# Performance work log

Hardware: AMD Instinct MI355X
Metric: run time of the kernel (lower is better)

## Reference

```python
import jax, jax.numpy as jnp
import numpy as np

B, S, H = 4, 4096, 256
WINDOW = 128


def setup_inputs() -> dict:
    key = jax.random.key(0)
    ks = jax.random.split(key, 7)
    s = 1.0 / np.sqrt(H)
    return {
        "x": jax.random.normal(ks[0], (B, S, H), dtype=jnp.float32),
        "Wq": jax.random.normal(ks[1], (H, H), dtype=jnp.float32) * s,
        "bq": jax.random.normal(ks[2], (H,), dtype=jnp.float32) * s,
        "Wk": jax.random.normal(ks[3], (H, H), dtype=jnp.float32) * s,
        "bk": jax.random.normal(ks[4], (H,), dtype=jnp.float32) * s,
        "Wv": jax.random.normal(ks[5], (H, H), dtype=jnp.float32) * s,
        "bv": jax.random.normal(ks[6], (H,), dtype=jnp.float32) * s,
        "window_size": WINDOW,
    }


def reference(x, Wq, bq, Wk, bk, Wv, bv, window_size):
    # x: [B, S, H]
    seq_len = x.shape[1]
    hidden = x.shape[2]
    scale = jnp.sqrt(jnp.asarray(hidden, dtype=x.dtype))
    q = jnp.einsum('bsh,hd->bsd', x, Wq) + bq
    k = jnp.einsum('bsh,hd->bsd', x, Wk) + bk
    v = jnp.einsum('bsh,hd->bsd', x, Wv) + bv
    scores = jnp.einsum('bsd,btd->bst', q, k) / scale  # [B, S, S]
    idx = jnp.arange(seq_len)
    band = jnp.abs(idx[:, None] - idx[None, :]) <= window_size  # [S, S]
    neg_inf = jnp.asarray(-jnp.inf, dtype=scores.dtype)
    scores = jnp.where(band[None, :, :], scores, neg_inf)
    weights = jax.nn.softmax(scores, axis=-1)
    context = jnp.einsum('bst,btd->bsd', weights, v)  # [B, S, H]
    return context.mean(axis=1)  # [B, H]
```

## Files before the change

### kernel.cpp

```cpp
#include <hip/hip_runtime.h>

#define SDIM 4096
#define HDIM 256
#define WIN 128
#define NROW 16384
#define QSCALE 0.0625f

typedef __attribute__((ext_vector_type(8))) short bf16x8;
typedef __attribute__((ext_vector_type(4))) float f32x4;

static __device__ __forceinline__ unsigned short f2bf(float f) {
  unsigned int u = __float_as_uint(f);
  return (unsigned short)((u + 0x7fffu + ((u >> 16) & 1u)) >> 16);
}

#define MFMA16(a, b, c) __builtin_amdgcn_mfma_f32_16x16x32_bf16((a), (b), (c), 0, 0, 0)


__global__ __launch_bounds__(256) void wconv(const float* __restrict__ Wq,
                                             const float* __restrict__ Wk,
                                             const float* __restrict__ Wv,
                                             unsigned short* __restrict__ Wp) {
  const int m = blockIdx.y, nt = blockIdx.x;
  const float* __restrict__ W = (m == 0) ? Wq : (m == 1) ? Wk : Wv;
  const int tid = threadIdx.x, lane = tid & 63, w = tid >> 6;
  const int l15 = lane & 15, g = lane >> 4;
#pragma unroll
  for (int half = 0; half < 2; ++half) {
    int kk = w * 2 + half;
    bf16x8 v;
#pragma unroll
    for (int j = 0; j < 8; ++j)
      v[j] = (short)f2bf(W[(size_t)(32 * kk + 8 * g + j) * HDIM + 16 * nt + l15]);
    *(bf16x8*)(Wp + ((size_t)(m * 16 + nt) * 8 + kk) * 512 + (size_t)lane * 8) = v;
  }
}

__global__ __launch_bounds__(256) void qkv_mfma(
    const float* __restrict__ x, const unsigned short* __restrict__ Wp,
    const float* __restrict__ bq, const float* __restrict__ bk,
    const float* __restrict__ bv, unsigned short* __restrict__ Qp,
    unsigned short* __restrict__ Kp, unsigned short* __restrict__ Vp) {
  __shared__ unsigned short st[32][264];
  const int tid = threadIdx.x;
  const int lane = tid & 63, w = tid >> 6;
  const int l15 = lane & 15, g = lane >> 4;
  const size_t rb = (size_t)blockIdx.x * 32;
#pragma unroll
  for (int it = 0; it < 8; ++it) {
    int u = it * 256 + tid;
    int r = u >> 6, c4 = (u & 63) << 2;
    float4 f = *(const float4*)(x + (rb + r) * HDIM + c4);
    st[r][c4 + 0] = f2bf(f.x);
    st[r][c4 + 1] = f2bf(f.y);
    st[r][c4 + 2] = f2bf(f.z);
    st[r][c4 + 3] = f2bf(f.w);
  }
  __syncthreads();
  bf16x8 a[2][8];
#pragma unroll
  for (int rtl = 0; rtl < 2; ++rtl)
#pragma unroll
    for (int kk = 0; kk < 8; ++kk)
      a[rtl][kk] = *(const bf16x8*)&st[16 * rtl + l15][32 * kk + 8 * g];
  __syncthreads();
  const int tg0 = blockIdx.x * 2;
  for (int m = 0; m < 3; ++m) {
    const unsigned short* Wm = Wp + (size_t)m * 65536;
    const float* bias = (m == 0) ? bq : (m == 1) ? bk : bv;
#pragma unroll
    for (int ntl = 0; ntl < 4; ++ntl) {
      const int nt = 4 * w + ntl;
      const unsigned short* wp_ = Wm + (size_t)nt * 4096 + (size_t)lane * 8;
      bf16x8 wf[8];
#pragma unroll
      for (int kk = 0; kk < 8; ++kk) wf[kk] = *(const bf16x8*)(wp_ + kk * 512);
      f32x4 a0 = {0.f, 0.f, 0.f, 0.f}, a1 = {0.f, 0.f, 0.f, 0.f};
#pragma unroll
      for (int kk = 0; kk < 8; ++kk) {
        a0 = MFMA16(a[0][kk], wf[kk], a0);
        a1 = MFMA16(a[1][kk], wf[kk], a1);
      }
      float bn = bias[nt * 16 + l15];
#pragma unroll
      for (int r = 0; r < 4; ++r) {
        st[4 * g + r][nt * 16 + l15] = f2bf(a0[r] + bn);
        st[16 + 4 * g + r][nt * 16 + l15] = f2bf(a1[r] + bn);
      }
    }
    __syncthreads();
    if (m < 2) {
      unsigned short* O = (m == 0 ? Qp : Kp);
#pragma unroll
      for (int it = 0; it < 4; ++it) {
        int u = it * 256 + tid;
        int ln = u & 63, kk = (u >> 6) & 7, tgl = u >> 9;
        int lg = ln >> 4, lc = ln & 15;
        bf16x8 vv = *(const bf16x8*)&st[16 * tgl + lc][32 * kk + 8 * lg];
        *(bf16x8*)(O + ((size_t)(tg0 + tgl) * 8 + kk) * 512 + (size_t)ln * 8) = vv;
      }
    } else {
#pragma unroll
      for (int it = 0; it < 4; ++it) {
        int u = it * 256 + tid;
        int lc = u & 15, gg = (u >> 4) & 1, dt = (u >> 5) & 15, tgl = u >> 9;
        bf16x8 vv;
#pragma unroll
        for (int j = 0; j < 8; ++j)
          vv[j] = (short)st[16 * tgl + 8 * gg + j][16 * dt + lc];
        *(bf16x8*)(Vp + (size_t)(tg0 + tgl) * 4096 +
                   (size_t)(dt * 32 + gg * 16 + lc) * 8) = vv;
      }
    }
    __syncthreads();
  }
}

__global__ __launch_bounds__(256) void attn_mfma(
    const unsigned short* __restrict__ Qp, const unsigned short* __restrict__ Kp,
    const unsigned short* __restrict__ Vp, float* __restrict__ partial) {
  __shared__ unsigned short plds[4][2][16][40];
  __shared__ float lsh[4][16];
  __shared__ float fbuf[4][256];
  const int tid = threadIdx.x;
  const int lane = tid & 63, w = tid >> 6;
  const int bid = blockIdx.x;
  const int blk = (bid & 7) * 128 + (bid >> 3);
  const int b = blk >> 8;
  const int qt = blk & 255;
  const int s0 = qt << 4;
  const int l15 = lane & 15, g = lane >> 4;
  bf16x8 qf[8];
  const unsigned short* qp_ = Qp + ((size_t)b * 256 + qt) * 4096 + (size_t)lane * 8;
#pragma unroll
  for (int kk = 0; kk < 8; ++kk) qf[kk] = *(const bf16x8*)(qp_ + kk * 512);
  const unsigned short* Kb = Kp + (size_t)b * 1048576;
  const unsigned short* Vb = Vp + (size_t)b * 1048576;
  f32x4 acc[16];
  const f32x4 zero = {0.f, 0.f, 0.f, 0.f};
#pragma unroll
  for (int i = 0; i < 16; ++i) acc[i] = zero;
  float lacc[4] = {0.f, 0.f, 0.f, 0.f};

  const int t0A = s0 - WIN + 64 * w;
  const int tgA = qt - 8 + 4 * w;
  const int tg0 = min(max(tgA + 0, 0), 255);
  const int tg1 = min(max(tgA + 1, 0), 255);
  const int tg2 = min(max(tgA + 2, 0), 255);
  const int tg3 = min(max(tgA + 3, 0), 255);
  const unsigned short* k0p = Kb + (size_t)tg0 * 4096 + (size_t)lane * 8;
  const unsigned short* k1p = Kb + (size_t)tg1 * 4096 + (size_t)lane * 8;
  const unsigned short* k2p = Kb + (size_t)tg2 * 4096 + (size_t)lane * 8;
  const unsigned short* k3p = Kb + (size_t)tg3 * 4096 + (size_t)lane * 8;
  f32x4 sc0 = zero, sc1 = zero, sc2 = zero, sc3 = zero;
#pragma unroll
  for (int kk = 0; kk < 8; ++kk) {
    sc0 = MFMA16(qf[kk], *(const bf16x8*)(k0p + kk * 512), sc0);
    sc1 = MFMA16(qf[kk], *(const bf16x8*)(k1p + kk * 512), sc1);
    sc2 = MFMA16(qf[kk], *(const bf16x8*)(k2p + kk * 512), sc2);
    sc3 = MFMA16(qf[kk], *(const bf16x8*)(k3p + kk * 512), sc3);
  }
  float p[4][4];
#pragma unroll
  for (int r = 0; r < 4; ++r) {
    const int s = s0 + 4 * g + r;
    const f32x4 sv[4] = {sc0, sc1, sc2, sc3};
#pragma unroll
    for (int ti = 0; ti < 4; ++ti) {
      int t = t0A + 16 * ti + l15;
      bool ok = (t >= 0) && (t < SDIM) && (t - s <= WIN) && (t - s >= -WIN);
      p[ti][r] = ok ? __expf(sv[ti][r] * QSCALE) : 0.f;
    }
  }
#pragma unroll
  for (int r = 0; r < 4; ++r) {
    float v = p[0][r] + p[1][r] + p[2][r] + p[3][r];
    v += __shfl_xor(v, 1);
    v += __shfl_xor(v, 2);
    v += __shfl_xor(v, 4);
    v += __shfl_xor(v, 8);
    lacc[r] += v;
  }
#pragma unroll
  for (int r = 0; r < 4; ++r) {
    plds[w][0][4 * g + r][l15] = f2bf(p[0][r]);
    plds[w][0][4 * g + r][16 + l15] = f2bf(p[1][r]);
    plds[w][1][4 * g + r][l15] = f2bf(p[2][r]);
    plds[w][1][4 * g + r][16 + l15] = f2bf(p[3][r]);
  }
  bf16x8 paA = *(const bf16x8*)&plds[w][0][l15][8 * g];
  bf16x8 paB = *(const bf16x8*)&plds[w][1][l15][8 * g];
  const int tgvA = min(max(tgA + (g >> 1), 0), 255);
  const int tgvB = min(max(tgA + 2 + (g >> 1), 0), 255);
  const unsigned short* vpA =
      Vb + (size_t)tgvA * 4096 + (size_t)(g & 1) * 128 + (size_t)l15 * 8;
  const unsigned short* vpB =
      Vb + (size_t)tgvB * 4096 + (size_t)(g & 1) * 128 + (size_t)l15 * 8;
#pragma unroll
  for (int dt = 0; dt < 16; ++dt) {
    acc[dt] = MFMA16(paA, *(const bf16x8*)(vpA + dt * 256), acc[dt]);
    acc[dt] = MFMA16(paB, *(const bf16x8*)(vpB + dt * 256), acc[dt]);
  }

  if (w == 3) {
    const int t0C = s0 + WIN;
    const int tgC = min(qt + 8, 255);
    const unsigned short* kcp = Kb + (size_t)tgC * 4096 + (size_t)lane * 8;
    f32x4 scC = zero;
#pragma unroll
    for (int kk = 0; kk < 8; ++kk)
      scC = MFMA16(qf[kk], *(const bf16x8*)(kcp + kk * 512), scC);
    float pC[4];
#pragma unroll
    for (int r = 0; r < 4; ++r) {
      int s = s0 + 4 * g + r;
      int t = t0C + l15;
      bool ok = (t < SDIM) && (t - s <= WIN);
      pC[r] = ok ? __expf(scC[r] * QSCALE) : 0.f;
      float v = pC[r];
      v += __shfl_xor(v, 1);
      v += __shfl_xor(v, 2);
      v += __shfl_xor(v, 4);
      v += __shfl_xor(v, 8);
      lacc[r] += v;
    }
#pragma unroll
    for (int r = 0; r < 4; ++r) {
      plds[w][0][4 * g + r][l15] = f2bf(pC[r]);
      plds[w][0][4 * g + r][16 + l15] = 0;
    }
    bf16x8 paC = *(const bf16x8*)&plds[w][0][l15][8 * g];
    const int tgvC = min(max(tgC + (g >> 1), 0), 255);
    const unsigned short* vpC =
        Vb + (size_t)tgvC * 4096 + (size_t)(g & 1) * 128 + (size_t)l15 * 8;
#pragma unroll
    for (int dt = 0; dt < 16; ++dt)
      acc[dt] = MFMA16(paC, *(const bf16x8*)(vpC + dt * 256), acc[dt]);
  }

  if (l15 == 0) {
#pragma unroll
    for (int r = 0; r < 4; ++r) lsh[w][4 * g + r] = lacc[r];
  }
  __syncthreads();
  float li[4];
#pragma unroll
  for (int r = 0; r < 4; ++r)
    li[r] = 1.0f / (lsh[0][4 * g + r] + lsh[1][4 * g + r] + lsh[2][4 * g + r] +
                    lsh[3][4 * g + r]);
#pragma unroll
  for (int dt = 0; dt < 16; ++dt) {
    float s = acc[dt][0] * li[0] + acc[dt][1] * li[1] + acc[dt][2] * li[2] +
              acc[dt][3] * li[3];
    s += __shfl_xor(s, 16);
    s += __shfl_xor(s, 32);
    if (lane < 16) fbuf[w][dt * 16 + lane] = s;
  }
  __syncthreads();
  partial[(size_t)blk * HDIM + tid] =
      fbuf[0][tid] + fbuf[1][tid] + fbuf[2][tid] + fbuf[3][tid];
}

__global__ __launch_bounds__(256) void reduce_partials(
    const float* __restrict__ partial, float* __restrict__ out) {
  __shared__ float red[16][17];
  const int cx = blockIdx.x, b = blockIdx.y;
  const int lc = threadIdx.x & 15, rg = threadIdx.x >> 4;
  float s = 0.f;
#pragma unroll
  for (int i = 0; i < 16; ++i)
    s += partial[((size_t)b * 256 + rg * 16 + i) * HDIM + cx * 16 + lc];
  red[rg][lc] = s;
  __syncthreads();
  if (rg == 0) {
    float t = 0.f;
#pragma unroll
    for (int r = 0; r < 16; ++r) t += red[r][lc];
    out[(size_t)b * HDIM + cx * 16 + lc] = t * (1.0f / (float)SDIM);
  }
}

extern "C" void kernel_launch(void* const* d_in, const int* in_sizes, int n_in,
                              void* d_out, int out_size, void* d_ws, size_t ws_size,
                              hipStream_t stream) {
  const float* x  = (const float*)d_in[0];
  const float* Wq = (const float*)d_in[1];
  const float* bq = (const float*)d_in[2];
  const float* Wk = (const float*)d_in[3];
  const float* bk = (const float*)d_in[4];
  const float* Wv = (const float*)d_in[5];
  const float* bv = (const float*)d_in[6];
  float* out = (float*)d_out;

  unsigned short* Wp = (unsigned short*)d_ws;
  unsigned short* Qp = Wp + 3 * 65536;
  unsigned short* Kp = Qp + (size_t)NROW * HDIM;
  unsigned short* Vp = Kp + (size_t)NROW * HDIM;
  float* partial = (float*)(Vp + (size_t)NROW * HDIM);

  dim3 wg(16, 3);
  wconv<<<wg, 256, 0, stream>>>(Wq, Wk, Wv, Wp);
  qkv_mfma<<<512, 256, 0, stream>>>(x, Wp, bq, bk, bv, Qp, Kp, Vp);
  attn_mfma<<<1024, 256, 0, stream>>>(Qp, Kp, Vp, partial);
  dim3 rg(16, 4);
  reduce_partials<<<rg, 256, 0, stream>>>(partial, out);
}
```

Baseline: 48.83 us.

## Fuse weight conversion into QKV kernel with flag-based inter-block sync

Removes the separate weight-conversion launch. The first 48 blocks of the QKV projection kernel now convert Wq/Wk/Wv to packed bf16 and publish completion flags with release atomics. Every block stages its x tile, then spin-waits on all 48 flags before reading the packed weights. Launch-bounds occupancy hints are also added to both kernels. The flags are never reset between calls, so later calls do not wait for fresh weights, and the spin-wait relies on the producer blocks being co-resident.

```diff
diff --git a/kernel.cpp b/kernel.cpp
--- a/kernel.cpp
+++ b/kernel.cpp
@@ -5,6 +5,7 @@
 #define WIN 128
 #define NROW 16384
 #define QSCALE 0.0625f
+#define MAGIC 0x7F3A9C51u
 
 typedef __attribute__((ext_vector_type(8))) short bf16x8;
 typedef __attribute__((ext_vector_type(4))) float f32x4;
@@ -17,35 +18,43 @@
 #define MFMA16(a, b, c) __builtin_amdgcn_mfma_f32_16x16x32_bf16((a), (b), (c), 0, 0, 0)
 
 
-__global__ __launch_bounds__(256) void wconv(const float* __restrict__ Wq,
-                                             const float* __restrict__ Wk,
-                                             const float* __restrict__ Wv,
-                                             unsigned short* __restrict__ Wp) {
-  const int m = blockIdx.y, nt = blockIdx.x;
-  const float* __restrict__ W = (m == 0) ? Wq : (m == 1) ? Wk : Wv;
-  const int tid = threadIdx.x, lane = tid & 63, w = tid >> 6;
-  const int l15 = lane & 15, g = lane >> 4;
-#pragma unroll
-  for (int half = 0; half < 2; ++half) {
-    int kk = w * 2 + half;
-    bf16x8 v;
-#pragma unroll
-    for (int j = 0; j < 8; ++j)
-      v[j] = (short)f2bf(W[(size_t)(32 * kk + 8 * g + j) * HDIM + 16 * nt + l15]);
-    *(bf16x8*)(Wp + ((size_t)(m * 16 + nt) * 8 + kk) * 512 + (size_t)lane * 8) = v;
-  }
-}
-
-__global__ __launch_bounds__(256) void qkv_mfma(
-    const float* __restrict__ x, const unsigned short* __restrict__ Wp,
-    const float* __restrict__ bq, const float* __restrict__ bk,
-    const float* __restrict__ bv, unsigned short* __restrict__ Qp,
-    unsigned short* __restrict__ Kp, unsigned short* __restrict__ Vp) {
+__global__ __launch_bounds__(256, 2) void qkv_mfma(
+    const float* __restrict__ x,
+    const float* __restrict__ Wq, const float* __restrict__ Wk,
+    const float* __restrict__ Wv, const float* __restrict__ bq,
+    const float* __restrict__ bk, const float* __restrict__ bv,
+    unsigned short* __restrict__ Wp, unsigned short* __restrict__ Qp,
+    unsigned short* __restrict__ Kp, unsigned short* __restrict__ Vp,
+    unsigned* __restrict__ sent) {
   __shared__ unsigned short st[32][264];
   const int tid = threadIdx.x;
   const int lane = tid & 63, w = tid >> 6;
   const int l15 = lane & 15, g = lane >> 4;
-  const size_t rb = (size_t)blockIdx.x * 32;
+  const int blk = blockIdx.x;
+
+  if (blk < 48) {
+    const int m = blk >> 4, nt = blk & 15;
+    const float* __restrict__ W = (m == 0) ? Wq : (m == 1) ? Wk : Wv;
+#pragma unroll
+    for (int it = 0; it < 2; ++it) {
+      int u = it * 256 + tid;
+      int kk = u >> 6, ln = u & 63;
+      int lg = ln >> 4, lc = ln & 15;
+      bf16x8 v;
+#pragma unroll
+      for (int j = 0; j < 8; ++j)
+        v[j] = (short)f2bf(W[(size_t)(32 * kk + 8 * lg + j) * HDIM + 16 * nt + lc]);
+      *(bf16x8*)(Wp + ((size_t)(m * 16 + nt) * 8 + kk) * 512 + (size_t)ln * 8) = v;
+    }
+    __syncthreads();
+    if (tid == 0) {
+      __threadfence();
+      __hip_atomic_store(sent + blk, MAGIC, __ATOMIC_RELEASE,
+                         __HIP_MEMORY_SCOPE_AGENT);
+    }
+  }
+
+  const size_t rb = (size_t)blk * 32;
 #pragma unroll
   for (int it = 0; it < 8; ++it) {
     int u = it * 256 + tid;
@@ -64,7 +73,15 @@
     for (int kk = 0; kk < 8; ++kk)
       a[rtl][kk] = *(const bf16x8*)&st[16 * rtl + l15][32 * kk + 8 * g];
   __syncthreads();
-  const int tg0 = blockIdx.x * 2;
+
+  if (tid < 48) {
+    while (__hip_atomic_load(sent + tid, __ATOMIC_ACQUIRE,
+                             __HIP_MEMORY_SCOPE_AGENT) != MAGIC)
+      __builtin_amdgcn_s_sleep(2);
+  }
+  __syncthreads();
+
+  const int tg0 = blk * 2;
   for (int m = 0; m < 3; ++m) {
     const unsigned short* Wm = Wp + (size_t)m * 65536;
     const float* bias = (m == 0) ? bq : (m == 1) ? bk : bv;
@@ -116,7 +133,7 @@
   }
 }
 
-__global__ __launch_bounds__(256) void attn_mfma(
+__global__ __launch_bounds__(256, 4) void attn_mfma(
     const unsigned short* __restrict__ Qp, const unsigned short* __restrict__ Kp,
     const unsigned short* __restrict__ Vp, float* __restrict__ partial) {
   __shared__ unsigned short plds[4][2][16][40];
@@ -297,10 +314,10 @@
   unsigned short* Kp = Qp + (size_t)NROW * HDIM;
   unsigned short* Vp = Kp + (size_t)NROW * HDIM;
   float* partial = (float*)(Vp + (size_t)NROW * HDIM);
-
-  dim3 wg(16, 3);
-  wconv<<<wg, 256, 0, stream>>>(Wq, Wk, Wv, Wp);
-  qkv_mfma<<<512, 256, 0, stream>>>(x, Wp, bq, bk, bv, Qp, Kp, Vp);
+  unsigned* sent = (unsigned*)(partial + (size_t)1024 * HDIM);
+
+  qkv_mfma<<<512, 256, 0, stream>>>(x, Wq, Wk, Wv, bq, bk, bv, Wp, Qp, Kp, Vp,
+                                    sent);
   attn_mfma<<<1024, 256, 0, stream>>>(Qp, Kp, Vp, partial);
   dim3 rg(16, 4);
   reduce_partials<<<rg, 256, 0, stream>>>(partial, out);
```

Result: slower. 50.50 us (+3.4%).
